# Kernel tuning notes

Measured on AMD Instinct MI355X. Metric: run time of the kernel, lower is better.

Reference implementation:

```python
import jax, jax.numpy as jnp
import numpy as np

B = 16384      # batch of Monte Carlo paths
N = 100        # time steps
DIM_W = 3
DT = 0.01
SQRT_DT = DT ** 0.5
SIGMA0 = 0.5   # constant diffusion coefficient (concrete sigma = SIGMA0 * ones(B,1,DIM_W))


def _mlp(x, W1, b1, W2, b2, W3, b3):
    h = jax.nn.relu(x @ W1 + b1)
    h = jax.nn.relu(h @ W2 + b2)
    return h @ W3 + b3


def setup_inputs() -> dict:
    key = jax.random.key(0)
    ks = jax.random.split(key, 8)
    s = 0.1  # modest weight scale for numerical sanity
    return {
        'y0': jnp.ones((1,), jnp.float32),
        'Y0': jnp.zeros((1, 1), jnp.float32),
        'zW1': s * jax.random.normal(ks[0], (2, 64), jnp.float32),
        'zb1': jnp.zeros((64,), jnp.float32),
        'zW2': s * jax.random.normal(ks[1], (64, 64), jnp.float32),
        'zb2': jnp.zeros((64,), jnp.float32),
        'zW3': s * jax.random.normal(ks[2], (64, 3), jnp.float32),
        'zb3': jnp.zeros((3,), jnp.float32),
        'qW1': s * jax.random.normal(ks[3], (2, 64), jnp.float32),
        'qb1': jnp.zeros((64,), jnp.float32),
        'qW2': s * jax.random.normal(ks[4], (64, 64), jnp.float32),
        'qb2': jnp.zeros((64,), jnp.float32),
        'qW3': s * jax.random.normal(ks[5], (64, 1), jnp.float32),
        'qb3': jnp.zeros((1,), jnp.float32),
        'dW': jax.random.normal(ks[6], (N, B, DIM_W), jnp.float32),
        'dZ': jax.random.normal(ks[7], (N, B, DIM_W), jnp.float32),
    }


def reference(y0, Y0, zW1, zb1, zW2, zb2, zW3, zb3,
              qW1, qb1, qW2, qb2, qW3, qb3, dW, dZ):
    y = jnp.broadcast_to(y0.reshape(1, 1), (B, 1))          # (B,1) state
    Y = jnp.broadcast_to(Y0, (B, 1))                         # (B,1) value process
    t = jnp.zeros((B, 1), jnp.float32)

    def step(carry, noise):
        y, Y, t, loss_acc = carry
        dWi, dZi = noise
        inp = jnp.concatenate([t, y], axis=1)                # (B,2)
        z = _mlp(inp, zW1, zb1, zW2, zb2, zW3, zb3)          # (B,3)
        q = _mlp(inp, qW1, qb1, qW2, qb2, qW3, qb3)          # (B,1)
        f = 0.5 * q * q                                      # generator (B,1)
        dw = dWi * SQRT_DT
        dz = dZi * SQRT_DT
        # sigma = SIGMA0 * ones(B,1,DIM_W); bmm(sigma, dw) = SIGMA0 * sum_j dw_j
        diffusion = SIGMA0 * jnp.sum(dw, axis=1, keepdims=True)
        y_new = y + q * DT + diffusion                       # mu = q
        Y_next = Y - f * DT + jnp.sum(z * dw, axis=1, keepdims=True)
        residual = Y_next - (Y - f * DT + jnp.sum(z * dz, axis=1, keepdims=True))
        loss_acc = loss_acc + jnp.mean(residual * residual)
        return (y_new, Y_next, t + DT, loss_acc), None

    (y, Y, t, total_residual_loss), _ = jax.lax.scan(
        step, (y, Y, t, jnp.float32(0.0)), (dW, dZ))
    terminal = y * y                                         # terminal_cost(y)
    terminal_loss = jnp.mean((Y - terminal) ** 2)
    return terminal_loss + total_residual_loss
```

## Files before the change

### kernel.cpp

```cpp
#include <hip/hip_runtime.h>
#include <hip/hip_bf16.h>

#define BATCH   16384
#define NSTEPS  100
#define DT_     0.01f
#define SQRTDT  0.1f
#define SIGMA0_ 0.5f

typedef _Float16  f16x2  __attribute__((ext_vector_type(2)));
typedef _Float16  f16x4  __attribute__((ext_vector_type(4)));
typedef _Float16  f16x8  __attribute__((ext_vector_type(8)));
typedef __fp16    h16x2  __attribute__((ext_vector_type(2)));
typedef float     f32x4  __attribute__((ext_vector_type(4)));

typedef const __attribute__((address_space(1))) void* gas_ptr;
typedef __attribute__((address_space(3))) void*       las_ptr;

__global__ void zero_out_kernel(float* out) { if (threadIdx.x == 0) out[0] = 0.0f; }

static __device__ __forceinline__ f16x4 pk4(const f32x4& d) {
    union { h16x2 h[2]; f16x4 v; } c;
    c.h[0] = __builtin_amdgcn_cvt_pkrtz(d[0], d[1]);
    c.h[1] = __builtin_amdgcn_cvt_pkrtz(d[2], d[3]);
    return c.v;
}

__launch_bounds__(256, 2)
__global__ void deepbsde_kernel(
    const float* __restrict__ y0,  const float* __restrict__ Y0,
    const float* __restrict__ zW1, const float* __restrict__ zb1,
    const float* __restrict__ zW2, const float* __restrict__ zb2,
    const float* __restrict__ zW3, const float* __restrict__ zb3,
    const float* __restrict__ qW1, const float* __restrict__ qb1,
    const float* __restrict__ qW2, const float* __restrict__ qb2,
    const float* __restrict__ qW3, const float* __restrict__ qb3,
    const float* __restrict__ dW,  const float* __restrict__ dZ,
    float* __restrict__ out)
{
    __shared__ __align__(16) char zring[2][8][384];
    __shared__ __align__(16) char qring[2][8][192];
    __shared__ __align__(16) _Float16 tbl[NSTEPS * 128];
    __shared__ float yring[2][8][16];
    __shared__ float ffin[2][16];
    __shared__ int   flags[2][2];

    const int tid  = threadIdx.x;
    const int lane = tid & 63;
    const int w    = tid >> 6;
    const int g    = w & 1;
    const bool isQ = (w >= 2);
    const int ln15 = lane & 15, q4 = lane >> 4;
    const int gw   = (blockIdx.x << 1) + g;
    const int pbase = gw << 4;

    if (tid < 4) ((int*)flags)[tid] = 0;

    auto fillz = [&](int i) {
        if (lane < 24) {
            const char* gp = (lane < 12)
                ? (const char*)dW + ((size_t)i * BATCH + pbase) * 12 + (size_t)lane * 16
                : (const char*)dZ + ((size_t)i * BATCH + pbase) * 12 + (size_t)(lane - 12) * 16;
            __builtin_amdgcn_global_load_lds((gas_ptr)gp, (las_ptr)&zring[g][i & 7][0],
                                             16, 0, 0);
        }
    };
    auto fillq = [&](int i) {
        if (lane < 12) {
            const char* gp = (const char*)dW + ((size_t)i * BATCH + pbase) * 12 + (size_t)lane * 16;
            __builtin_amdgcn_global_load_lds((gas_ptr)gp, (las_ptr)&qring[g][i & 7][0],
                                             16, 0, 0);
        }
    };
    if (!isQ) { fillz(0); fillz(1); fillz(2); fillz(3); }
    else      { fillq(0); fillq(1); fillq(2); fillq(3); }

    {
        float tt = 0.0f;
        for (int i = 0; i < NSTEPS; ++i) {
            int r = (tid - (i << 6)) & 255;
            if (r < 64) {
                int q4e = r >> 4, mlp = (r >> 3) & 1, m = r & 7;
                const float* Wp = mlp ? qW1 : zW1;
                const float* bp = mlp ? qb1 : zb1;
                int i0 = 2*m, i1 = 2*m + 1;
                int k0 = 32*(i0 >> 3) + 8*q4e + (i0 & 7);
                int k1 = 32*(i1 >> 3) + 8*q4e + (i1 & 7);
                _Float16 th = (_Float16)tt;
                f16x2 A = {(_Float16)Wp[k0], (_Float16)Wp[k1]};
                f16x2 C = {(_Float16)bp[k0], (_Float16)bp[k1]};
                f16x2 tv = {th, th};
                f16x2 v = A*tv + C;
                int idx = (i*4 + q4e)*16 + mlp*8 + m;
                *(f16x2*)&tbl[idx << 1] = v;
            }
            tt += DT_;
        }
    }

    const float* W1p = isQ ? qW1 : zW1;
    const float* W2p = isQ ? qW2 : zW2;
    const float* b2p = isQ ? qb2 : zb2;

    f16x2 B1[8];
#pragma unroll
    for (int m = 0; m < 8; ++m) {
        int i0 = 2*m, i1 = 2*m + 1;
        int k0 = 32*(i0 >> 3) + 8*q4 + (i0 & 7);
        int k1 = 32*(i1 >> 3) + 8*q4 + (i1 & 7);
        B1[m] = (f16x2){(_Float16)W1p[64 + k0], (_Float16)W1p[64 + k1]};
    }

    f16x8 Af[4][2];
#pragma unroll
    for (int tN = 0; tN < 4; ++tN)
#pragma unroll
        for (int f = 0; f < 2; ++f)
#pragma unroll
            for (int j = 0; j < 8; ++j) {
                int k = 32*f + 8*q4 + j, n = 16*tN + ln15;
                Af[tN][f][j] = (_Float16)W2p[k*64 + n];
            }

    f32x4 b2v[4];
#pragma unroll
    for (int tN = 0; tN < 4; ++tN)
#pragma unroll
        for (int r = 0; r < 4; ++r)
            b2v[tN][r] = b2p[16*tN + 4*q4 + r];

    const int c3 = ln15 & 3;
    f16x8 A3[2];
#pragma unroll
    for (int fl = 0; fl < 2; ++fl)
#pragma unroll
        for (int j = 0; j < 8; ++j) {
            int tN = 2*fl + (j >> 2);
            int n  = 16*tN + 4*q4 + (j & 3);
            float wv = isQ ? ((c3 == 3) ? qW3[n]                 : 0.0f)
                           : ((c3 < 3)  ? SQRTDT * zW3[n*3 + c3] : 0.0f);
            A3[fl][j] = (_Float16)wv;
        }

    const f32x4 C3b = isQ ? (f32x4){0.0f, 0.0f, 0.0f, qb3[0]}
                          : (f32x4){SQRTDT*zb3[0], SQRTDT*zb3[1], SQRTDT*zb3[2], 0.0f};

    const float CSIG = SIGMA0_ * SQRTDT;
    const float NHDT = -0.5f * DT_;
    const float y0v = y0[0], Y0v = Y0[0];

    const f16x2 zero2h = {(_Float16)0.0f, (_Float16)0.0f};
    const f16x4 zero4h = {(_Float16)0.0f, (_Float16)0.0f, (_Float16)0.0f, (_Float16)0.0f};

    auto mlp = [&](float ycur, f16x8 t0, f16x8 t1) -> f32x4 {
        _Float16 yh = (_Float16)ycur;
        const f16x2 yv = {yh, yh};
        union U8 { f16x8 v; f16x2 h[4]; };
        U8 T0; T0.v = t0; U8 T1; T1.v = t1;
        union { f16x2 h[4]; f16x8 v; } b0, b1;
#pragma unroll
        for (int m = 0; m < 4; ++m) {
            b0.h[m] = __builtin_elementwise_max((f16x2)(B1[m]*yv   + T0.h[m]), zero2h);
            b1.h[m] = __builtin_elementwise_max((f16x2)(B1[m+4]*yv + T1.h[m]), zero2h);
        }
        union { f16x4 q[4]; f16x8 o[2]; } Bh;
#pragma unroll
        for (int tN = 0; tN < 4; ++tN) {
            f32x4 d = b2v[tN];
            d = __builtin_amdgcn_mfma_f32_16x16x32_f16(Af[tN][0], b0.v, d, 0, 0, 0);
            d = __builtin_amdgcn_mfma_f32_16x16x32_f16(Af[tN][1], b1.v, d, 0, 0, 0);
            Bh.q[tN] = __builtin_elementwise_max(pk4(d), zero4h);
        }
        f32x4 Pv = C3b;
        Pv = __builtin_amdgcn_mfma_f32_16x16x32_f16(A3[0], Bh.o[0], Pv, 0, 0, 0);
        Pv = __builtin_amdgcn_mfma_f32_16x16x32_f16(A3[1], Bh.o[1], Pv, 0, 0, 0);
        return Pv;
    };

    __syncthreads();

    f16x8 c0, c1, d0, d1;

    if (!isQ) {
        float y = y0v, Ysum = 0.0f, acc = 0.0f;
        { const f16x8* tp = (const f16x8*)(tbl + q4*32); c0 = tp[0]; c1 = tp[1]; }

        auto zbody = [&](int i, f16x8& t0, f16x8& t1, f16x8& u0, f16x8& u1) {
            const float* sl = (const float*)&zring[g][i & 7][0];
            float nw0 = sl[ln15*3 + 0], nw1 = sl[ln15*3 + 1], nw2 = sl[ln15*3 + 2];
            float nz0 = sl[48 + ln15*3 + 0], nz1 = sl[48 + ln15*3 + 1], nz2 = sl[48 + ln15*3 + 2];
            int ip = i + 1; ip = (ip > NSTEPS - 1) ? NSTEPS - 1 : ip;
            { const f16x8* tp = (const f16x8*)(tbl + (ip*4 + q4)*32); u0 = tp[0]; u1 = tp[1]; }

            f32x4 P = mlp(y, t0, t1);
            float zs0 = P[0], zs1 = P[1], zs2 = P[2];
            float zdw = fmaf(zs2, nw2, fmaf(zs1, nw1, zs0*nw0));
            float zdz = fmaf(zs2, nz2, fmaf(zs1, nz1, zs0*nz0));
            Ysum += zdw;
            float r = zdw - zdz;
            acc = fmaf(r, r, acc);

            volatile int* qf = &flags[g][0];
            while (*qf < i + 1) { }
            y = *(volatile float*)&yring[g][(i + 1) & 7][ln15];
            if (lane == 0) *(volatile int*)&flags[g][1] = i + 1;
        };

#pragma unroll 1
        for (int i = 0; i < NSTEPS - 4; i += 2) {
            __builtin_amdgcn_s_waitcnt(0x0F73);
            fillz(i + 4);
            zbody(i,     c0, c1, d0, d1);
            __builtin_amdgcn_s_waitcnt(0x0F73);
            fillz(i + 5);
            zbody(i + 1, d0, d1, c0, c1);
        }
        __builtin_amdgcn_s_waitcnt(0x0F70);
        zbody(NSTEPS - 4, c0, c1, d0, d1);
        zbody(NSTEPS - 3, d0, d1, c0, c1);
        zbody(NSTEPS - 2, c0, c1, d0, d1);
        zbody(NSTEPS - 1, d0, d1, c0, c1);

        {
            volatile int* qf = &flags[g][0];
            while (*qf < NSTEPS + 1) { }
        }
        float Fq  = *(volatile float*)&ffin[g][ln15];
        float Yvf = Y0v + Fq + Ysum;
        float dterm = Yvf - y*y;
        acc = fmaf(dterm, dterm, acc);

        float val = (q4 == 0) ? acc : 0.0f;
#pragma unroll
        for (int off = 1; off < 64; off <<= 1) val += __shfl_xor(val, off);
        if (lane == 0) atomicAdd(out, val * (1.0f / BATCH));
    } else {
        float y = y0v, Facc = 0.0f;
        { const f16x8* tp = (const f16x8*)(tbl + q4*32); c0 = tp[2]; c1 = tp[3]; }

        auto qbody = [&](int j, f16x8& t0, f16x8& t1, f16x8& u0, f16x8& u1) {
            const float* sl = (const float*)&qring[g][j & 7][0];
            float nw0 = sl[ln15*3 + 0], nw1 = sl[ln15*3 + 1], nw2 = sl[ln15*3 + 2];

            f32x4 P = mlp(y, t0, t1);
            float qv = P[3];

            if (j >= 6) {
                volatile int* zp = &flags[g][1];
                while (*zp < j - 5) { }
            }

            float snw = (nw0 + nw1) + nw2;
            Facc = fmaf(NHDT*qv, qv, Facc);
            y = fmaf(CSIG, snw, fmaf(qv, DT_, y));

            if (q4 == 0) *(volatile float*)&yring[g][(j + 1) & 7][ln15] = y;
            __builtin_amdgcn_s_waitcnt(0xC07F);
            if (lane == 0) *(volatile int*)&flags[g][0] = j + 1;

            int jp = j + 1; jp = (jp > NSTEPS - 1) ? NSTEPS - 1 : jp;
            { const f16x8* tp = (const f16x8*)(tbl + (jp*4 + q4)*32); u0 = tp[2]; u1 = tp[3]; }
        };

#pragma unroll 1
        for (int j = 0; j < NSTEPS - 4; j += 2) {
            __builtin_amdgcn_s_waitcnt(0x0F73);
            fillq(j + 4);
            qbody(j,     c0, c1, d0, d1);
            __builtin_amdgcn_s_waitcnt(0x0F73);
            fillq(j + 5);
            qbody(j + 1, d0, d1, c0, c1);
        }
        __builtin_amdgcn_s_waitcnt(0x0F70);
        qbody(NSTEPS - 4, c0, c1, d0, d1);
        qbody(NSTEPS - 3, d0, d1, c0, c1);
        qbody(NSTEPS - 2, c0, c1, d0, d1);
        qbody(NSTEPS - 1, d0, d1, c0, c1);

        if (q4 == 0) *(volatile float*)&ffin[g][ln15] = Facc;
        __builtin_amdgcn_s_waitcnt(0xC07F);
        if (lane == 0) *(volatile int*)&flags[g][0] = NSTEPS + 1;
    }
}

extern "C" void kernel_launch(void* const* d_in, const int* in_sizes, int n_in,
                              void* d_out, int out_size, void* d_ws, size_t ws_size,
                              hipStream_t stream)
{
    zero_out_kernel<<<1, 64, 0, stream>>>((float*)d_out);
    deepbsde_kernel<<<512, 256, 0, stream>>>(
        (const float*)d_in[0],  (const float*)d_in[1],
        (const float*)d_in[2],  (const float*)d_in[3],
        (const float*)d_in[4],  (const float*)d_in[5],
        (const float*)d_in[6],  (const float*)d_in[7],
        (const float*)d_in[8],  (const float*)d_in[9],
        (const float*)d_in[10], (const float*)d_in[11],
        (const float*)d_in[12], (const float*)d_in[13],
        (const float*)d_in[14], (const float*)d_in[15],
        (float*)d_out);
}
```

Measured before the change: 165.2 us.

## Batch z/q wavefront handshakes every four steps using a full y history buffer

The q-MLP wavefronts now write every step's y into a buffer sized for all steps and publish a progress flag only once per four steps. The backpressure wait on the z wavefronts is removed. The z wavefronts spin once per four steps and read four y values together, so fewer LDS spin-polls and flag stores sit on the critical path. In exchange, yring LDS grows to the full step count, and the z side can trail the q side by up to four steps.

```diff
diff --git a/kernel.cpp b/kernel.cpp
--- a/kernel.cpp
+++ b/kernel.cpp
@@ -40,7 +40,7 @@
     __shared__ __align__(16) char zring[2][8][384];
     __shared__ __align__(16) char qring[2][8][192];
     __shared__ __align__(16) _Float16 tbl[NSTEPS * 128];
-    __shared__ float yring[2][8][16];
+    __shared__ float yring[2][NSTEPS + 1][16];
     __shared__ float ffin[2][16];
     __shared__ int   flags[2][2];
 
@@ -79,9 +79,9 @@
         for (int i = 0; i < NSTEPS; ++i) {
             int r = (tid - (i << 6)) & 255;
             if (r < 64) {
-                int q4e = r >> 4, mlp = (r >> 3) & 1, m = r & 7;
-                const float* Wp = mlp ? qW1 : zW1;
-                const float* bp = mlp ? qb1 : zb1;
+                int q4e = r >> 4, mlp_ = (r >> 3) & 1, m = r & 7;
+                const float* Wp = mlp_ ? qW1 : zW1;
+                const float* bp = mlp_ ? qb1 : zb1;
                 int i0 = 2*m, i1 = 2*m + 1;
                 int k0 = 32*(i0 >> 3) + 8*q4e + (i0 & 7);
                 int k1 = 32*(i1 >> 3) + 8*q4e + (i1 & 7);
@@ -90,7 +90,7 @@
                 f16x2 C = {(_Float16)bp[k0], (_Float16)bp[k1]};
                 f16x2 tv = {th, th};
                 f16x2 v = A*tv + C;
-                int idx = (i*4 + q4e)*16 + mlp*8 + m;
+                int idx = (i*4 + q4e)*16 + mlp_*8 + m;
                 *(f16x2*)&tbl[idx << 1] = v;
             }
             tt += DT_;
@@ -181,44 +181,65 @@
     f16x8 c0, c1, d0, d1;
 
     if (!isQ) {
-        float y = y0v, Ysum = 0.0f, acc = 0.0f;
+        float Ysum = 0.0f, acc = 0.0f;
+        float ya, yb, yc, yd;
         { const f16x8* tp = (const f16x8*)(tbl + q4*32); c0 = tp[0]; c1 = tp[1]; }
 
-        auto zbody = [&](int i, f16x8& t0, f16x8& t1, f16x8& u0, f16x8& u1) {
+        auto zbody = [&](int i, float ycur, f16x8& t0, f16x8& t1, f16x8& u0, f16x8& u1) {
             const float* sl = (const float*)&zring[g][i & 7][0];
             float nw0 = sl[ln15*3 + 0], nw1 = sl[ln15*3 + 1], nw2 = sl[ln15*3 + 2];
             float nz0 = sl[48 + ln15*3 + 0], nz1 = sl[48 + ln15*3 + 1], nz2 = sl[48 + ln15*3 + 2];
             int ip = i + 1; ip = (ip > NSTEPS - 1) ? NSTEPS - 1 : ip;
             { const f16x8* tp = (const f16x8*)(tbl + (ip*4 + q4)*32); u0 = tp[0]; u1 = tp[1]; }
 
-            f32x4 P = mlp(y, t0, t1);
+            f32x4 P = mlp(ycur, t0, t1);
             float zs0 = P[0], zs1 = P[1], zs2 = P[2];
             float zdw = fmaf(zs2, nw2, fmaf(zs1, nw1, zs0*nw0));
             float zdz = fmaf(zs2, nz2, fmaf(zs1, nz1, zs0*nz0));
             Ysum += zdw;
             float r = zdw - zdz;
             acc = fmaf(r, r, acc);
-
+        };
+        auto ybatch = [&](int base) {
             volatile int* qf = &flags[g][0];
-            while (*qf < i + 1) { }
-            y = *(volatile float*)&yring[g][(i + 1) & 7][ln15];
-            if (lane == 0) *(volatile int*)&flags[g][1] = i + 1;
+            while (*qf < base + 4) { }
+            ya = *(volatile float*)&yring[g][base + 1][ln15];
+            yb = *(volatile float*)&yring[g][base + 2][ln15];
+            yc = *(volatile float*)&yring[g][base + 3][ln15];
+            yd = *(volatile float*)&yring[g][base + 4][ln15];
         };
 
+        __builtin_amdgcn_s_waitcnt(0x0F73); fillz(4);
+        zbody(0, y0v, c0, c1, d0, d1);
+        ybatch(0);
 #pragma unroll 1
-        for (int i = 0; i < NSTEPS - 4; i += 2) {
-            __builtin_amdgcn_s_waitcnt(0x0F73);
-            fillz(i + 4);
-            zbody(i,     c0, c1, d0, d1);
-            __builtin_amdgcn_s_waitcnt(0x0F73);
-            fillz(i + 5);
-            zbody(i + 1, d0, d1, c0, c1);
-        }
+        for (int b = 0; b < 23; ++b) {
+            int i = 4*b;
+            __builtin_amdgcn_s_waitcnt(0x0F73); fillz(i + 5);
+            zbody(i + 1, ya, d0, d1, c0, c1);
+            __builtin_amdgcn_s_waitcnt(0x0F73); fillz(i + 6);
+            zbody(i + 2, yb, c0, c1, d0, d1);
+            __builtin_amdgcn_s_waitcnt(0x0F73); fillz(i + 7);
+            zbody(i + 3, yc, d0, d1, c0, c1);
+            __builtin_amdgcn_s_waitcnt(0x0F73); fillz(i + 8);
+            zbody(i + 4, yd, c0, c1, d0, d1);
+            ybatch(i + 4);
+        }
+        __builtin_amdgcn_s_waitcnt(0x0F73); fillz(97);
+        zbody(93, ya, d0, d1, c0, c1);
+        __builtin_amdgcn_s_waitcnt(0x0F73); fillz(98);
+        zbody(94, yb, c0, c1, d0, d1);
+        __builtin_amdgcn_s_waitcnt(0x0F73); fillz(99);
+        zbody(95, yc, d0, d1, c0, c1);
+        __builtin_amdgcn_s_waitcnt(0x0F73);
+        zbody(96, yd, c0, c1, d0, d1);
+        ybatch(96);
+        __builtin_amdgcn_s_waitcnt(0x0F72);
+        zbody(97, ya, d0, d1, c0, c1);
+        __builtin_amdgcn_s_waitcnt(0x0F71);
+        zbody(98, yb, c0, c1, d0, d1);
         __builtin_amdgcn_s_waitcnt(0x0F70);
-        zbody(NSTEPS - 4, c0, c1, d0, d1);
-        zbody(NSTEPS - 3, d0, d1, c0, c1);
-        zbody(NSTEPS - 2, c0, c1, d0, d1);
-        zbody(NSTEPS - 1, d0, d1, c0, c1);
+        zbody(99, yc, d0, d1, c0, c1);
 
         {
             volatile int* qf = &flags[g][0];
@@ -226,7 +247,8 @@
         }
         float Fq  = *(volatile float*)&ffin[g][ln15];
         float Yvf = Y0v + Fq + Ysum;
-        float dterm = Yvf - y*y;
+        float yT  = yd;
+        float dterm = Yvf - yT*yT;
         acc = fmaf(dterm, dterm, acc);
 
         float val = (q4 == 0) ? acc : 0.0f;
@@ -240,41 +262,41 @@
         auto qbody = [&](int j, f16x8& t0, f16x8& t1, f16x8& u0, f16x8& u1) {
             const float* sl = (const float*)&qring[g][j & 7][0];
             float nw0 = sl[ln15*3 + 0], nw1 = sl[ln15*3 + 1], nw2 = sl[ln15*3 + 2];
+            int jp = j + 1; jp = (jp > NSTEPS - 1) ? NSTEPS - 1 : jp;
+            { const f16x8* tp = (const f16x8*)(tbl + (jp*4 + q4)*32); u0 = tp[2]; u1 = tp[3]; }
 
             f32x4 P = mlp(y, t0, t1);
             float qv = P[3];
-
-            if (j >= 6) {
-                volatile int* zp = &flags[g][1];
-                while (*zp < j - 5) { }
-            }
-
             float snw = (nw0 + nw1) + nw2;
             Facc = fmaf(NHDT*qv, qv, Facc);
             y = fmaf(CSIG, snw, fmaf(qv, DT_, y));
-
-            if (q4 == 0) *(volatile float*)&yring[g][(j + 1) & 7][ln15] = y;
+            if (q4 == 0) *(volatile float*)&yring[g][j + 1][ln15] = y;
+        };
+
+#pragma unroll 1
+        for (int jb = 0; jb < 24; ++jb) {
+            int j = 4*jb;
+            __builtin_amdgcn_s_waitcnt(0x0F73); fillq(j + 4);
+            qbody(j,     c0, c1, d0, d1);
+            __builtin_amdgcn_s_waitcnt(0x0F73); fillq(j + 5);
+            qbody(j + 1, d0, d1, c0, c1);
+            __builtin_amdgcn_s_waitcnt(0x0F73); fillq(j + 6);
+            qbody(j + 2, c0, c1, d0, d1);
+            __builtin_amdgcn_s_waitcnt(0x0F73); fillq(j + 7);
+            qbody(j + 3, d0, d1, c0, c1);
             __builtin_amdgcn_s_waitcnt(0xC07F);
-            if (lane == 0) *(volatile int*)&flags[g][0] = j + 1;
-
-            int jp = j + 1; jp = (jp > NSTEPS - 1) ? NSTEPS - 1 : jp;
-            { const f16x8* tp = (const f16x8*)(tbl + (jp*4 + q4)*32); u0 = tp[2]; u1 = tp[3]; }
-        };
-
-#pragma unroll 1
-        for (int j = 0; j < NSTEPS - 4; j += 2) {
-            __builtin_amdgcn_s_waitcnt(0x0F73);
-            fillq(j + 4);
-            qbody(j,     c0, c1, d0, d1);
-            __builtin_amdgcn_s_waitcnt(0x0F73);
-            fillq(j + 5);
-            qbody(j + 1, d0, d1, c0, c1);
-        }
+            if (lane == 0) *(volatile int*)&flags[g][0] = j + 4;
+        }
+        __builtin_amdgcn_s_waitcnt(0x0F73);
+        qbody(96, c0, c1, d0, d1);
+        __builtin_amdgcn_s_waitcnt(0x0F72);
+        qbody(97, d0, d1, c0, c1);
+        __builtin_amdgcn_s_waitcnt(0x0F71);
+        qbody(98, c0, c1, d0, d1);
         __builtin_amdgcn_s_waitcnt(0x0F70);
-        qbody(NSTEPS - 4, c0, c1, d0, d1);
-        qbody(NSTEPS - 3, d0, d1, c0, c1);
-        qbody(NSTEPS - 2, c0, c1, d0, d1);
-        qbody(NSTEPS - 1, d0, d1, c0, c1);
+        qbody(99, d0, d1, c0, c1);
+        __builtin_amdgcn_s_waitcnt(0xC07F);
+        if (lane == 0) *(volatile int*)&flags[g][0] = NSTEPS;
 
         if (q4 == 0) *(volatile float*)&ffin[g][ln15] = Facc;
         __builtin_amdgcn_s_waitcnt(0xC07F);
```

Result: faster. 155.2 us (-6.0%).
